# Kernel tuning notes

Hardware: AMD Instinct MI355X
Metric: run time of the kernel (lower is better)

Reference implementation:

```python
import jax, jax.numpy as jnp
import numpy as np

IN, H, OUT = 512, 1024, 256
ODE_UNFOLDS = 6
EPS = 1e-08


def setup_inputs() -> dict:
    key = jax.random.key(0)
    ks = jax.random.split(key, 12)
    B, S = 64, 256
    inp = {
        "x": jax.random.normal(ks[0], (B, S, IN), dtype=jnp.float32),
        "h0": jnp.zeros((B, H), dtype=jnp.float32),
        "timespans": jnp.ones((B, S), dtype=jnp.float32),
        # parameters (nn.Linear default-style init scales)
        "tau": jax.random.uniform(ks[1], (H,), minval=1.0, maxval=100.0, dtype=jnp.float32),
        "W_in_w": jax.random.normal(ks[2], (H, IN), dtype=jnp.float32) / np.sqrt(IN),
        "W_in_b": jax.random.normal(ks[3], (H,), dtype=jnp.float32) / np.sqrt(IN),
        "W_rec_w": jax.random.normal(ks[4], (H, H), dtype=jnp.float32) / np.sqrt(H),
        "wiring_mask": jnp.ones((H, H), dtype=jnp.float32),  # AUTO_NCP -> else branch -> ones
        "W_out_w": jax.random.normal(ks[5], (OUT, H), dtype=jnp.float32) / np.sqrt(H),
        "W_out_b": jax.random.normal(ks[6], (OUT,), dtype=jnp.float32) / np.sqrt(H),
        "alpha": jnp.ones((H,), dtype=jnp.float32) * 0.9,
        "beta": jnp.ones((H,), dtype=jnp.float32),
        "mu": jnp.zeros((H,), dtype=jnp.float32),
        "sigma": jnp.ones((H,), dtype=jnp.float32),
    }
    return inp


def reference(x, h0, timespans, tau, W_in_w, W_in_b, W_rec_w, wiring_mask,
              W_out_w, W_out_b, alpha, beta, mu, sigma):
    # masked recurrent weight (constant across time, hoisted out of the loop)
    w_rec = W_rec_w * wiring_mask  # (H, H)

    def time_step(h, inp):
        x_t, dt = inp  # x_t: (B, IN), dt: (B, 1)
        i_in = x_t @ W_in_w.T + W_in_b  # constant across unfolds for this t
        d = dt / ODE_UNFOLDS

        def unfold(h, _):
            i_rec = h @ w_rec.T  # (B, H)
            f = jax.nn.sigmoid((i_rec - mu) / (sigma + EPS))
            dhdt = -alpha * h + beta * f * (i_in + i_rec)
            return h + d * dhdt / tau, None

        h, _ = jax.lax.scan(unfold, h, None, length=ODE_UNFOLDS)
        y_t = h @ W_out_w.T + W_out_b  # (B, OUT)
        return h, y_t

    xs = (jnp.swapaxes(x, 0, 1), jnp.swapaxes(timespans, 0, 1)[..., None])  # (S,B,IN),(S,B,1)
    h_final, ys = jax.lax.scan(time_step, h0, xs)  # ys: (S, B, OUT)
    output = jnp.swapaxes(ys, 0, 1)  # (B, S, OUT)
    return output, h_final
```

## Files before the change

### kernel.cpp

```cpp
#include <hip/hip_runtime.h>

#define IN_DIM   512
#define H_DIM    1024
#define OUT_DIM  256
#define B_DIM    64
#define S_DIM    256
#define EPS_F    1e-8f

#define BPG      4
#define JPW      64
#define NTHREADS 512
#define NWG      256
#define SLOT_STRIDE 65536

#define OUT_Y_TOTAL ((size_t)B_DIM*S_DIM*OUT_DIM)

typedef float    f32x4 __attribute__((ext_vector_type(4)));
typedef unsigned u32x4 __attribute__((ext_vector_type(4)));
typedef short    s16x8 __attribute__((ext_vector_type(8)));

#define MFMA16 __builtin_amdgcn_mfma_f32_16x16x32_bf16

union B8 { unsigned u[4]; s16x8 v; };

__device__ __forceinline__ s16x8 round_bf16x8(f32x4 f0, f32x4 f1) {
  B8 H;
  float fv[8];
#pragma unroll
  for (int e = 0; e < 4; ++e) { fv[e] = f0[e]; fv[e+4] = f1[e]; }
#pragma unroll
  for (int d = 0; d < 4; ++d) {
    unsigned u0 = __float_as_uint(fv[2*d])   + 0x8000u;
    unsigned u1 = __float_as_uint(fv[2*d+1]) + 0x8000u;
    H.u[d] = (u0 >> 16) | (u1 & 0xFFFF0000u);
  }
  return H.v;
}

__device__ __forceinline__ void split_bf16(f32x4 f0, f32x4 f1, s16x8* hi, s16x8* lo) {
  B8 H, L;
  float fv[8];
#pragma unroll
  for (int e = 0; e < 4; ++e) { fv[e] = f0[e]; fv[e+4] = f1[e]; }
#pragma unroll
  for (int d = 0; d < 4; ++d) {
    unsigned u0 = __float_as_uint(fv[2*d]);
    unsigned u1 = __float_as_uint(fv[2*d+1]);
    unsigned t0 = u0 & 0xffff0000u, t1 = u1 & 0xffff0000u;
    H.u[d] = (u0 >> 16) | t1;
    L.u[d] = ((__float_as_uint(fv[2*d]   - __uint_as_float(t0))) >> 16)
           | ((__float_as_uint(fv[2*d+1] - __uint_as_float(t1))) & 0xffff0000u);
  }
  *hi = H.v; *lo = L.v;
}

__device__ __forceinline__ unsigned dec_tag(u32x4 q) {
  return (q.x & 7u) | ((q.y & 7u) << 3) | ((q.z & 7u) << 6) | ((q.w & 7u) << 9);
}
__device__ __forceinline__ s16x8 pack_hi(u32x4 a, u32x4 b) {
  B8 t;
  t.u[0] = (a.y & 0xFFFF0000u) | (a.x >> 16);
  t.u[1] = (a.w & 0xFFFF0000u) | (a.z >> 16);
  t.u[2] = (b.y & 0xFFFF0000u) | (b.x >> 16);
  t.u[3] = (b.w & 0xFFFF0000u) | (b.z >> 16);
  return t.v;
}
__device__ __forceinline__ s16x8 pack_lo(u32x4 a, u32x4 b) {
  B8 t;
  t.u[0] = ((a.y & 0xFFF8u) << 16) | (a.x & 0xFFF8u);
  t.u[1] = ((a.w & 0xFFF8u) << 16) | (a.z & 0xFFF8u);
  t.u[2] = ((b.y & 0xFFF8u) << 16) | (b.x & 0xFFF8u);
  t.u[3] = ((b.w & 0xFFF8u) << 16) | (b.z & 0xFFF8u);
  return t.v;
}

#define POLL_BODY(FLAGS)                                                      \
  asm volatile(                                                               \
    "global_load_dwordx4 %0, %8, off " FLAGS "\n\t"                           \
    "global_load_dwordx4 %1, %8, off offset:16 " FLAGS "\n\t"                 \
    "global_load_dwordx4 %2, %8, off offset:128 " FLAGS "\n\t"                \
    "global_load_dwordx4 %3, %8, off offset:144 " FLAGS "\n\t"                \
    "global_load_dwordx4 %4, %8, off offset:256 " FLAGS "\n\t"                \
    "global_load_dwordx4 %5, %8, off offset:272 " FLAGS "\n\t"                \
    "global_load_dwordx4 %6, %8, off offset:384 " FLAGS "\n\t"                \
    "global_load_dwordx4 %7, %8, off offset:400 " FLAGS "\n\t"                \
    "s_waitcnt vmcnt(0)"                                                      \
    : "=&v"(q0), "=&v"(q1), "=&v"(q2), "=&v"(q3),                             \
      "=&v"(q4), "=&v"(q5), "=&v"(q6), "=&v"(q7)                              \
    : "v"(ap) : "memory")

__global__ void __launch_bounds__(NTHREADS)
ltc_kernel(const float* __restrict__ x, const float* __restrict__ h0,
           const float* __restrict__ tspan, const float* __restrict__ tau,
           const float* __restrict__ Wiw, const float* __restrict__ Wib,
           const float* __restrict__ Wrw, const float* __restrict__ wmask,
           const float* __restrict__ Wow, const float* __restrict__ Wob,
           const float* __restrict__ alpha_p, const float* __restrict__ beta_p,
           const float* __restrict__ mu_p, const float* __restrict__ sigma_p,
           float* __restrict__ out, unsigned* __restrict__ hb)
{
  __shared__ float sch[2][8][4][68];
  __shared__ float scx[8][4][68];
  __shared__ float scy[8][4][20];
  __shared__ char lds_pad[57344];

  const int tid = threadIdx.x;
  ((volatile char*)lds_pad)[tid] = 0;

  const int wg  = blockIdx.x;
  const int g   = wg >> 4;
  const int w   = wg & 15;
  const int b0g = g * BPG;
  const int jw0 = w * JPW;
  const int l   = tid & 63;
  const int v   = tid >> 6;
  const int vb  = v & 3;
  const int gb_e = b0g + vb;
  const int gj  = jw0 + l;

  s16x8 wbh[4][4];
#pragma unroll
  for (int i = 0; i < 4; ++i) {
    const int k0 = v*128 + i*32 + ((l >> 4) << 3);
#pragma unroll
    for (int nt = 0; nt < 4; ++nt) {
      const size_t go = (size_t)(jw0 + nt*16 + (l & 15))*H_DIM + k0;
      f32x4 w0 = *(const f32x4*)(Wrw + go)     * *(const f32x4*)(wmask + go);
      f32x4 w1 = *(const f32x4*)(Wrw + go + 4) * *(const f32x4*)(wmask + go + 4);
      wbh[i][nt] = round_bf16x8(w0, w1);
    }
  }

  const float mu_s  = mu_p[gj];
  const float sgi_s = 1.0f / (sigma_p[gj] + EPS_F);
  const float al_s  = alpha_p[gj];
  const float be_s  = beta_p[gj];
  const float ti_s  = 1.0f / tau[gj];
  const float wib_s = Wib[gj];
  float hold_s = h0[((size_t)gb_e << 10) + gj];
  float tsc = tspan[(size_t)gb_e*S_DIM] * (1.0f/6.0f);

  auto store_h = [&](float hn, unsigned slot, unsigned tag) {
    unsigned uh = __float_as_uint(hn) & 0xFFFF0000u;
    float r = hn - __uint_as_float(uh);
    unsigned e = (uh | (__float_as_uint(r) >> 16)) & ~7u;
    e |= (tag >> (3*(l & 3))) & 7u;
    unsigned* dst = hb + slot*SLOT_STRIDE + ((unsigned)gb_e << 10) + (unsigned)gj;
    asm volatile("global_store_dword %0, %1, off sc0 sc1"
                 :: "v"(dst), "v"(e) : "memory");
  };

  if (v < 4) store_h(hold_s, 0u, 0u);

  auto acquire = [&](unsigned slotC, unsigned tagC,
                     u32x4& q0, u32x4& q1, u32x4& q2, u32x4& q3,
                     u32x4& q4, u32x4& q5, u32x4& q6, u32x4& q7) {
    const unsigned* ap = hb + slotC*SLOT_STRIDE
                       + ((unsigned)(b0g + (l & 15)) << 10)
                       + (unsigned)(v*128 + ((l >> 4) << 3));
    for (;;) {
      int ok;
      if ((l & 15) < 4) {
        POLL_BODY("sc0 sc1");
        ok = (dec_tag(q0) == tagC) & (dec_tag(q1) == tagC) &
             (dec_tag(q2) == tagC) & (dec_tag(q3) == tagC) &
             (dec_tag(q4) == tagC) & (dec_tag(q5) == tagC) &
             (dec_tag(q6) == tagC) & (dec_tag(q7) == tagC);
      } else ok = 1;
      if (__all(ok)) break;
      __builtin_amdgcn_s_sleep(1);
    }
  };

  auto iin_partials = [&](int tt, f32x4 ax[4]) {
    const int r = l & 15, c = (l >> 4) << 3;
    const float* xp = x + ((size_t)(b0g + (r & 3))*S_DIM + tt)*IN_DIM + v*64 + c;
    f32x4 xq0 = *(const f32x4*)xp,        xq1 = *(const f32x4*)(xp + 4);
    f32x4 xq2 = *(const f32x4*)(xp + 32), xq3 = *(const f32x4*)(xp + 36);
#pragma unroll
    for (int i2 = 0; i2 < 2; ++i2) {
      s16x8 xh, xl;
      split_bf16(i2 ? xq2 : xq0, i2 ? xq3 : xq1, &xh, &xl);
#pragma unroll
      for (int nt = 0; nt < 4; ++nt) {
        const float* wp = Wiw + (size_t)(jw0 + nt*16 + (l & 15))*IN_DIM + v*64 + i2*32 + c;
        s16x8 wh = round_bf16x8(*(const f32x4*)wp, *(const f32x4*)(wp + 4));
        ax[nt] = MFMA16(xh, wh, ax[nt], 0,0,0);
        ax[nt] = MFMA16(xl, wh, ax[nt], 0,0,0);
      }
    }
  };

  auto load_wout = [&](s16x8 woY[4]) {
#pragma unroll
    for (int i = 0; i < 4; ++i) {
      const int k0 = v*128 + i*32 + ((l >> 4) << 3);
      const size_t go = (size_t)(w*16 + (l & 15))*H_DIM + k0;
      woY[i] = round_bf16x8(*(const f32x4*)(Wow + go), *(const f32x4*)(Wow + go + 4));
    }
  };

  float iin4 = 0.f, iin_nx = 0.f;
  {
    f32x4 ax[4] = {{0,0,0,0},{0,0,0,0},{0,0,0,0},{0,0,0,0}};
    iin_partials(0, ax);
    if (l < 16) {
#pragma unroll
      for (int nt = 0; nt < 4; ++nt)
#pragma unroll
        for (int q = 0; q < 4; ++q) scx[v][q][nt*16 + l] = ax[nt][q];
    }
    __syncthreads();
    if (v < 4) {
      float s = wib_s;
#pragma unroll
      for (int kp = 0; kp < 8; ++kp) s += scx[kp][vb][l];
      iin4 = s;
    }
    __syncthreads();
  }

  unsigned p = 1;
#pragma unroll 1
  for (int t = 0; t < S_DIM; ++t) {
#pragma unroll 1
    for (int u = 0; u < 6; ++u, ++p) {
      const unsigned slotC = (p-1) & 1, tagC = (p-1) & 0xFFFu;
      const unsigned slotP = p & 1,     tagP = p & 0xFFFu;
      const bool doY = (u == 0);
      const bool doX = (u == 3) && (t + 1 < S_DIM);

      s16x8 woY[4];
      if (doY) load_wout(woY);

      u32x4 q0,q1,q2,q3,q4,q5,q6,q7;
      acquire(slotC, tagC, q0,q1,q2,q3,q4,q5,q6,q7);

      f32x4 acc[4] = {{0,0,0,0},{0,0,0,0},{0,0,0,0},{0,0,0,0}};
      f32x4 accy = {0.f,0.f,0.f,0.f};
#pragma unroll
      for (int i = 0; i < 4; ++i) {
        u32x4 qa = (i==0) ? q0 : (i==1) ? q2 : (i==2) ? q4 : q6;
        u32x4 qb = (i==0) ? q1 : (i==1) ? q3 : (i==2) ? q5 : q7;
        s16x8 ah = pack_hi(qa, qb), al = pack_lo(qa, qb);
#pragma unroll
        for (int nt = 0; nt < 4; ++nt) {
          acc[nt] = MFMA16(ah, wbh[i][nt], acc[nt], 0,0,0);
          acc[nt] = MFMA16(al, wbh[i][nt], acc[nt], 0,0,0);
        }
        if (doY) {
          accy = MFMA16(ah, woY[i], accy, 0,0,0);
          accy = MFMA16(al, woY[i], accy, 0,0,0);
        }
      }
      f32x4 ax[4] = {{0,0,0,0},{0,0,0,0},{0,0,0,0},{0,0,0,0}};
      if (doX) iin_partials(t + 1, ax);

      if (l < 16) {
#pragma unroll
        for (int nt = 0; nt < 4; ++nt)
#pragma unroll
          for (int q = 0; q < 4; ++q) sch[slotP][v][q][nt*16 + l] = acc[nt][q];
        if (doX) {
#pragma unroll
          for (int nt = 0; nt < 4; ++nt)
#pragma unroll
            for (int q = 0; q < 4; ++q) scx[v][q][nt*16 + l] = ax[nt][q];
        }
        if (doY) {
#pragma unroll
          for (int q = 0; q < 4; ++q) scy[v][q][l] = accy[q];
        }
      }
      __syncthreads();

      if (v < 4) {
        float ir = 0.f;
#pragma unroll
        for (int kp = 0; kp < 8; ++kp) ir += sch[slotP][kp][vb][l];
        const float z  = (ir - mu_s) * sgi_s;
        const float f  = 1.0f / (1.0f + __expf(-z));
        const float dh = -al_s*hold_s + be_s*f*(iin4 + ir);
        const float hn = hold_s + tsc*dh*ti_s;
        hold_s = hn;
        store_h(hn, slotP, tagP);
        if (doX) {
          float s = wib_s;
#pragma unroll
          for (int kp = 0; kp < 8; ++kp) s += scx[kp][vb][l];
          iin_nx = s;
        }
        if (u == 5) {
          if (t + 1 < S_DIM) {
            tsc = tspan[(size_t)gb_e*S_DIM + t + 1] * (1.0f/6.0f);
            iin4 = iin_nx;
          } else {
            out[OUT_Y_TOTAL + ((size_t)gb_e << 10) + gj] = hn;
          }
        }
      } else if (v == 4 && doY && t > 0) {
        const int b = l >> 4, oc = l & 15;
        float s = Wob[w*16 + oc];
#pragma unroll
        for (int kp = 0; kp < 8; ++kp) s += scy[kp][b][oc];
        out[((size_t)(b0g + b)*S_DIM + (t-1))*OUT_DIM + w*16 + oc] = s;
      }
    }
  }

  {
    const unsigned slotC = (p-1) & 1, tagC = (p-1) & 0xFFFu;
    s16x8 woY[4];
    load_wout(woY);
    u32x4 q0,q1,q2,q3,q4,q5,q6,q7;
    acquire(slotC, tagC, q0,q1,q2,q3,q4,q5,q6,q7);
    f32x4 accy = {0.f,0.f,0.f,0.f};
#pragma unroll
    for (int i = 0; i < 4; ++i) {
      u32x4 qa = (i==0) ? q0 : (i==1) ? q2 : (i==2) ? q4 : q6;
      u32x4 qb = (i==0) ? q1 : (i==1) ? q3 : (i==2) ? q5 : q7;
      s16x8 ah = pack_hi(qa, qb), al = pack_lo(qa, qb);
      accy = MFMA16(ah, woY[i], accy, 0,0,0);
      accy = MFMA16(al, woY[i], accy, 0,0,0);
    }
    if (l < 16) {
#pragma unroll
      for (int q = 0; q < 4; ++q) scy[v][q][l] = accy[q];
    }
    __syncthreads();
    if (v == 4) {
      const int b = l >> 4, oc = l & 15;
      float s = Wob[w*16 + oc];
#pragma unroll
      for (int kp = 0; kp < 8; ++kp) s += scy[kp][b][oc];
      out[((size_t)(b0g + b)*S_DIM + (S_DIM-1))*OUT_DIM + w*16 + oc] = s;
    }
  }
}

extern "C" void kernel_launch(void* const* d_in, const int* in_sizes, int n_in,
                              void* d_out, int out_size, void* d_ws, size_t ws_size,
                              hipStream_t stream) {
  const float* x    = (const float*)d_in[0];
  const float* h0   = (const float*)d_in[1];
  const float* ts   = (const float*)d_in[2];
  const float* tau  = (const float*)d_in[3];
  const float* Wiw  = (const float*)d_in[4];
  const float* Wib  = (const float*)d_in[5];
  const float* Wrw  = (const float*)d_in[6];
  const float* msk  = (const float*)d_in[7];
  const float* Wow  = (const float*)d_in[8];
  const float* Wob  = (const float*)d_in[9];
  const float* alp  = (const float*)d_in[10];
  const float* bet  = (const float*)d_in[11];
  const float* mu   = (const float*)d_in[12];
  const float* sg   = (const float*)d_in[13];
  float* out = (float*)d_out;
  unsigned* hb = (unsigned*)d_ws;

  hipMemsetAsync(hb, 0xFF, 2*SLOT_STRIDE*sizeof(unsigned), stream);

  void* args[] = { (void*)&x, (void*)&h0, (void*)&ts, (void*)&tau,
                   (void*)&Wiw, (void*)&Wib, (void*)&Wrw, (void*)&msk,
                   (void*)&Wow, (void*)&Wob, (void*)&alp, (void*)&bet,
                   (void*)&mu, (void*)&sg, (void*)&out, (void*)&hb };
  hipLaunchCooperativeKernel((const void*)ltc_kernel, dim3(NWG), dim3(NTHREADS),
                             args, 0, stream);
}
```

Before: 5.574 ms.

## Cache bf16 W_in tiles in LDS and split flag polling into two phases

Converts each workgroup's W_in slice to bf16 once at kernel start and keeps it in LDS, replacing the LDS padding array. The per-timestep input projection then reads these tiles instead of reloading and rounding fp32 weights from global memory. The acquire loop now polls two representative 16-byte chunks first and fetches the remaining six only after those tags match, which cuts coherent load traffic while spinning. The LDS allocation goes from 56 KB to 64 KB, which still keeps one workgroup per CU.

```diff
diff --git a/kernel.cpp b/kernel.cpp
--- a/kernel.cpp
+++ b/kernel.cpp
@@ -73,21 +73,6 @@
   t.u[3] = ((b.w & 0xFFF8u) << 16) | (b.z & 0xFFF8u);
   return t.v;
 }
-
-#define POLL_BODY(FLAGS)                                                      \
-  asm volatile(                                                               \
-    "global_load_dwordx4 %0, %8, off " FLAGS "\n\t"                           \
-    "global_load_dwordx4 %1, %8, off offset:16 " FLAGS "\n\t"                 \
-    "global_load_dwordx4 %2, %8, off offset:128 " FLAGS "\n\t"                \
-    "global_load_dwordx4 %3, %8, off offset:144 " FLAGS "\n\t"                \
-    "global_load_dwordx4 %4, %8, off offset:256 " FLAGS "\n\t"                \
-    "global_load_dwordx4 %5, %8, off offset:272 " FLAGS "\n\t"                \
-    "global_load_dwordx4 %6, %8, off offset:384 " FLAGS "\n\t"                \
-    "global_load_dwordx4 %7, %8, off offset:400 " FLAGS "\n\t"                \
-    "s_waitcnt vmcnt(0)"                                                      \
-    : "=&v"(q0), "=&v"(q1), "=&v"(q2), "=&v"(q3),                             \
-      "=&v"(q4), "=&v"(q5), "=&v"(q6), "=&v"(q7)                              \
-    : "v"(ap) : "memory")
 
 __global__ void __launch_bounds__(NTHREADS)
 ltc_kernel(const float* __restrict__ x, const float* __restrict__ h0,
@@ -102,11 +87,9 @@
   __shared__ float sch[2][8][4][68];
   __shared__ float scx[8][4][68];
   __shared__ float scy[8][4][20];
-  __shared__ char lds_pad[57344];
+  __shared__ __align__(16) char winlds[65536];
 
   const int tid = threadIdx.x;
-  ((volatile char*)lds_pad)[tid] = 0;
-
   const int wg  = blockIdx.x;
   const int g   = wg >> 4;
   const int w   = wg & 15;
@@ -131,6 +114,16 @@
     }
   }
 
+#pragma unroll
+  for (int i2 = 0; i2 < 2; ++i2)
+#pragma unroll
+    for (int nt = 0; nt < 4; ++nt) {
+      const float* wp = Wiw + (size_t)(jw0 + nt*16 + (l & 15))*IN_DIM
+                      + v*64 + i2*32 + ((l >> 4) << 3);
+      s16x8 wh = round_bf16x8(*(const f32x4*)wp, *(const f32x4*)(wp + 4));
+      *(s16x8*)(winlds + ((v*2 + i2)*4 + nt)*1024 + l*16) = wh;
+    }
+
   const float mu_s  = mu_p[gj];
   const float sgi_s = 1.0f / (sigma_p[gj] + EPS_F);
   const float al_s  = alpha_p[gj];
@@ -161,11 +154,31 @@
     for (;;) {
       int ok;
       if ((l & 15) < 4) {
-        POLL_BODY("sc0 sc1");
-        ok = (dec_tag(q0) == tagC) & (dec_tag(q1) == tagC) &
-             (dec_tag(q2) == tagC) & (dec_tag(q3) == tagC) &
-             (dec_tag(q4) == tagC) & (dec_tag(q5) == tagC) &
-             (dec_tag(q6) == tagC) & (dec_tag(q7) == tagC);
+        asm volatile(
+          "global_load_dwordx4 %0, %2, off sc0 sc1\n\t"
+          "global_load_dwordx4 %1, %2, off offset:256 sc0 sc1\n\t"
+          "s_waitcnt vmcnt(0)"
+          : "=&v"(q0), "=&v"(q4) : "v"(ap) : "memory");
+        ok = (dec_tag(q0) == tagC) & (dec_tag(q4) == tagC);
+      } else ok = 1;
+      if (__all(ok)) break;
+      __builtin_amdgcn_s_sleep(1);
+    }
+    for (;;) {
+      int ok;
+      if ((l & 15) < 4) {
+        asm volatile(
+          "global_load_dwordx4 %0, %6, off offset:16 sc0 sc1\n\t"
+          "global_load_dwordx4 %1, %6, off offset:128 sc0 sc1\n\t"
+          "global_load_dwordx4 %2, %6, off offset:144 sc0 sc1\n\t"
+          "global_load_dwordx4 %3, %6, off offset:272 sc0 sc1\n\t"
+          "global_load_dwordx4 %4, %6, off offset:384 sc0 sc1\n\t"
+          "global_load_dwordx4 %5, %6, off offset:400 sc0 sc1\n\t"
+          "s_waitcnt vmcnt(0)"
+          : "=&v"(q1), "=&v"(q2), "=&v"(q3), "=&v"(q5), "=&v"(q6), "=&v"(q7)
+          : "v"(ap) : "memory");
+        ok = (dec_tag(q1) == tagC) & (dec_tag(q2) == tagC) & (dec_tag(q3) == tagC) &
+             (dec_tag(q5) == tagC) & (dec_tag(q6) == tagC) & (dec_tag(q7) == tagC);
       } else ok = 1;
       if (__all(ok)) break;
       __builtin_amdgcn_s_sleep(1);
@@ -183,8 +196,7 @@
       split_bf16(i2 ? xq2 : xq0, i2 ? xq3 : xq1, &xh, &xl);
 #pragma unroll
       for (int nt = 0; nt < 4; ++nt) {
-        const float* wp = Wiw + (size_t)(jw0 + nt*16 + (l & 15))*IN_DIM + v*64 + i2*32 + c;
-        s16x8 wh = round_bf16x8(*(const f32x4*)wp, *(const f32x4*)(wp + 4));
+        s16x8 wh = *(const s16x8*)(winlds + ((v*2 + i2)*4 + nt)*1024 + l*16);
         ax[nt] = MFMA16(xh, wh, ax[nt], 0,0,0);
         ax[nt] = MFMA16(xl, wh, ax[nt], 0,0,0);
       }
```

After: 4.756 ms. 1.17x faster.
